# Performance work log

Measured on AMD Instinct MI355X. Metric: run time of the kernel, lower is better.

The kernel has to match this reference:

```python
import jax, jax.numpy as jnp
import numpy as np

N_EMBD = 768
N_HEAD = 12
HEAD_DIM = N_EMBD // N_HEAD


def setup_inputs() -> dict:
    key = jax.random.key(0)
    k1, k2, k3 = jax.random.split(key, 3)
    B, T = 8, 1024
    x = jax.random.normal(k1, (B, T, N_EMBD), dtype=jnp.float32)
    # torch Linear(n_embd, 3*n_embd, bias=False): y = x @ W^T; we store W_attn as (C, 3C)
    w_attn = jax.random.normal(k2, (N_EMBD, 3 * N_EMBD), dtype=jnp.float32) * (1.0 / np.sqrt(N_EMBD))
    w_proj = jax.random.normal(k3, (N_EMBD, N_EMBD), dtype=jnp.float32) * (1.0 / np.sqrt(N_EMBD))
    return {"x": x, "w_attn": w_attn, "w_proj": w_proj}


def reference(x, w_attn, w_proj):
    B, T, C = x.shape
    qkv = x @ w_attn                      # [B, T, 3C]
    q, k, v = jnp.split(qkv, 3, axis=-1)  # each [B, T, C]
    # [B, H, T, D]
    q = q.reshape(B, T, N_HEAD, HEAD_DIM).transpose(0, 2, 1, 3)
    k = k.reshape(B, T, N_HEAD, HEAD_DIM).transpose(0, 2, 1, 3)
    v = v.reshape(B, T, N_HEAD, HEAD_DIM).transpose(0, 2, 1, 3)
    scale = 1.0 / np.sqrt(HEAD_DIM)
    att = jnp.einsum('bhqd,bhkd->bhqk', q, k) * scale  # [B, H, T, T]
    causal = jnp.tril(jnp.ones((T, T), dtype=bool))
    att = jnp.where(causal[None, None, :, :], att, jnp.float32(-jnp.inf))
    att = jax.nn.softmax(att, axis=-1)
    # dropout disabled (eval / p=0.0) for deterministic reference
    y = jnp.einsum('bhqk,bhkd->bhqd', att, v)          # [B, H, T, D]
    y = y.transpose(0, 2, 1, 3).reshape(B, T, C)
    return y @ w_proj
```

## Files before the change

### kernel.cpp

```cpp
#include <hip/hip_runtime.h>
#include <hip/hip_bf16.h>
#include <math.h>

constexpr int Bz = 8;
constexpr int Tt = 1024;
constexpr int Cc = 768;
constexpr int Hh = 12;
constexpr int Dd = 64;
constexpr int BT = Bz * Tt;
constexpr int C3 = 3 * Cc;

using bf16x8 = __attribute__((ext_vector_type(8))) short;
using bf16x4 = __attribute__((ext_vector_type(4))) short;
using u16x8  = __attribute__((ext_vector_type(8))) unsigned short;
using f32x4  = __attribute__((ext_vector_type(4))) float;

__device__ __forceinline__ unsigned short f2bf(float f) {
  unsigned int u = __builtin_bit_cast(unsigned int, f);
  u += 0x7fffu + ((u >> 16) & 1u);
  return (unsigned short)(u >> 16);
}
__device__ __forceinline__ short f2bf_hw(float f) {
  __hip_bfloat16 h = __float2bfloat16(f);
  return __builtin_bit_cast(short, h);
}
__device__ __forceinline__ float fast_exp2(float x) {
#if __has_builtin(__builtin_amdgcn_exp2f)
  return __builtin_amdgcn_exp2f(x);
#else
  return exp2f(x);
#endif
}
__device__ __forceinline__ f32x4 mfma16_bf16(bf16x4 a, bf16x4 b, f32x4 c) {
#if __has_builtin(__builtin_amdgcn_mfma_f32_16x16x16bf16_1k)
  return __builtin_amdgcn_mfma_f32_16x16x16bf16_1k(a, b, c, 0, 0, 0);
#else
  asm volatile("v_mfma_f32_16x16x16_bf16 %0, %1, %2, %0" : "+v"(c) : "v"(a), "v"(b));
  return c;
#endif
}
__device__ __forceinline__ void stage16(const unsigned short* g, unsigned short* l) {
  __builtin_amdgcn_global_load_lds(
      (const __attribute__((address_space(1))) void*)g,
      (__attribute__((address_space(3))) void*)l, 16, 0, 0);
}

__global__ __launch_bounds__(256) void xcast_kernel(
    const float* __restrict__ in, unsigned short* __restrict__ out) {
  const size_t i = ((size_t)blockIdx.x * 256 + threadIdx.x) * 8;
  const float4 a = *(const float4*)(in + i);
  const float4 b = *(const float4*)(in + i + 4);
  u16x8 w;
  w[0] = f2bf(a.x); w[1] = f2bf(a.y); w[2] = f2bf(a.z); w[3] = f2bf(a.w);
  w[4] = f2bf(b.x); w[5] = f2bf(b.y); w[6] = f2bf(b.z); w[7] = f2bf(b.w);
  *(u16x8*)(out + i) = w;
}

__global__ __launch_bounds__(256) void tcast_kernel(
    const float* __restrict__ in, unsigned short* __restrict__ out, int K, int N) {
  __shared__ float t[32][33];
  const int tx = threadIdx.x, ty = threadIdx.y;
  const int kb = blockIdx.y * 32, nb = blockIdx.x * 32;
#pragma unroll
  for (int i = 0; i < 4; ++i)
    t[ty + 8 * i][tx] = in[(size_t)(kb + ty + 8 * i) * N + nb + tx];
  __syncthreads();
#pragma unroll
  for (int i = 0; i < 4; ++i)
    out[(size_t)(nb + ty + 8 * i) * K + kb + tx] = f2bf(t[tx][ty + 8 * i]);
}

#define GEMM_CORE_PROLOGUE()                                                   \
  __shared__ unsigned short As[128 * 32];                                      \
  __shared__ unsigned short Bs[128 * 32];                                      \
  const int tid = threadIdx.x;                                                 \
  const int wave = tid >> 6, lane = tid & 63;                                  \
  const int wr = wave >> 1, wc = wave & 1;                                     \
  const int lr = lane & 15;                                                    \
  const int lg = lane >> 4;                                                    \
  const int lrow = lane >> 2;                                                  \
  const int lcol = (lane & 3) * 8;                                             \
  const int brow = blockIdx.y * 128, bcol = blockIdx.x * 128;                  \
  f32x4 acc[4][4] = {};                                                        \
  for (int kt = 0; kt < K / 32; ++kt) {                                        \
    const int k0 = kt * 32;                                                    \
    __syncthreads();                                                           \
    _Pragma("unroll")                                                          \
    for (int i = 0; i < 2; ++i) {                                              \
      const int chunk = wave * 2 + i;                                          \
      const int row = chunk * 16 + lrow;                                       \
      stage16(A + (size_t)(brow + row) * K + k0 + lcol, &As[chunk * 512]);     \
      stage16(Bt + (size_t)(bcol + row) * K + k0 + lcol, &Bs[chunk * 512]);    \
    }                                                                          \
    __syncthreads();                                                           \
    bf16x8 af[4], bfr[4];                                                      \
    _Pragma("unroll")                                                          \
    for (int f = 0; f < 4; ++f) {                                              \
      af[f]  = *(const bf16x8*)&As[(wr * 64 + f * 16 + lr) * 32 + lg * 8];     \
      bfr[f] = *(const bf16x8*)&Bs[(wc * 64 + f * 16 + lr) * 32 + lg * 8];     \
    }                                                                          \
    _Pragma("unroll")                                                          \
    for (int fi = 0; fi < 4; ++fi)                                             \
      _Pragma("unroll")                                                        \
      for (int fj = 0; fj < 4; ++fj)                                           \
        acc[fi][fj] = __builtin_amdgcn_mfma_f32_16x16x32_bf16(                 \
            af[fi], bfr[fj], acc[fi][fj], 0, 0, 0);                            \
  }

__global__ __launch_bounds__(256) void gemm_qkv_kernel(
    const unsigned short* __restrict__ A, const unsigned short* __restrict__ Bt,
    unsigned short* __restrict__ qh, unsigned short* __restrict__ kh,
    unsigned short* __restrict__ vtg) {
  const int K = Cc;
  GEMM_CORE_PROLOGUE()

  const int region = bcol / Cc;
  const int nb = bcol - region * Cc;
#pragma unroll
  for (int fi = 0; fi < 4; ++fi) {
    const int m0 = brow + wr * 64 + fi * 16 + lg * 4;
    const int b_ = m0 >> 10, t0 = m0 & 1023;
#pragma unroll
    for (int fj = 0; fj < 4; ++fj) {
      const int n = nb + wc * 64 + fj * 16 + lr;
      const int h_ = n >> 6, d_ = n & 63;
      if (region < 2) {
        unsigned short* dst = (region == 0 ? qh : kh) +
            (((size_t)(b_ * Hh + h_)) * Tt + t0) * Dd + d_;
#pragma unroll
        for (int r = 0; r < 4; ++r) dst[(size_t)r * Dd] = f2bf(acc[fi][fj][r]);
      } else {
        ushort4 w;
        w.x = f2bf(acc[fi][fj][0]);
        w.y = f2bf(acc[fi][fj][1]);
        w.z = f2bf(acc[fi][fj][2]);
        w.w = f2bf(acc[fi][fj][3]);
        *(ushort4*)(vtg + (((size_t)(b_ * Hh + h_)) * Dd + d_) * Tt + t0) = w;
      }
    }
  }
}

__global__ __launch_bounds__(256) void gemm_bt_kernel(
    const unsigned short* __restrict__ A, const unsigned short* __restrict__ Bt,
    float* __restrict__ Cm, int M, int N, int K) {
  GEMM_CORE_PROLOGUE()

#pragma unroll
  for (int fi = 0; fi < 4; ++fi) {
    const size_t rbase = (size_t)(brow + wr * 64 + fi * 16 + lg * 4);
#pragma unroll
    for (int fj = 0; fj < 4; ++fj) {
      const int cbase = bcol + wc * 64 + fj * 16 + lr;
#pragma unroll
      for (int r = 0; r < 4; ++r)
        Cm[(rbase + r) * N + cbase] = acc[fi][fj][r];
    }
  }
}

__global__ __launch_bounds__(512, 4) void attn_mfma3_kernel(
    const unsigned short* __restrict__ qh, const unsigned short* __restrict__ kh,
    const unsigned short* __restrict__ vtg, unsigned short* __restrict__ y) {
  const int qtile = (Tt / 128 - 1) - blockIdx.x;
  const int h = blockIdx.y;
  const int b = blockIdx.z;
  const int qbase = qtile * 128;

  const int tid = threadIdx.x;
  const int wave = tid >> 6, lane = tid & 63;
  const int lr = lane & 15;
  const int lg = lane >> 4;

  __shared__ unsigned short Ks[128][72];
  __shared__ unsigned short Vt[64][136];

  const size_t head = ((size_t)(b * Hh + h)) * (Tt * Dd);
  const int qrow = qbase + wave * 16 + lr;

  bf16x8 qf0, qf1;
  {
    const unsigned short* qp = qh + head + (size_t)qrow * Dd;
    qf0 = *(const bf16x8*)(qp + lg * 8);
    qf1 = *(const bf16x8*)(qp + 32 + lg * 8);
  }

  f32x4 o[4] = {};
  float m_run = -INFINITY;
  float l_run = 0.0f;

  constexpr float kS = 0.125f * 1.4426950408889634f;
  const int lastT = qtile;

  {
    const unsigned short* kp = kh + head;
    const unsigned short* vp = vtg + head;
#pragma unroll
    for (int it = 0; it < 2; ++it) {
      const int s = tid + 512 * it;
      *(u16x8*)&Ks[s >> 3][(s & 7) * 8] =
          *(const u16x8*)(kp + (size_t)(s >> 3) * Dd + (s & 7) * 8);
      *(u16x8*)&Vt[s >> 4][(s & 15) * 8] =
          *(const u16x8*)(vp + (size_t)(s >> 4) * Tt + (s & 15) * 8);
    }
  }
  __syncthreads();

  for (int kt2 = 0; kt2 <= lastT; ++kt2) {
    const int kbase = kt2 * 128;
    const bool diagt = (kt2 == lastT);

    f32x4 sT[8];
#pragma unroll
    for (int jk = 0; jk < 8; ++jk) {
      if (!diagt || jk <= wave) {
        const bf16x8 kf0 = *(const bf16x8*)&Ks[jk * 16 + lr][lg * 8];
        const bf16x8 kf1 = *(const bf16x8*)&Ks[jk * 16 + lr][32 + lg * 8];
        f32x4 t = {};
        t = __builtin_amdgcn_mfma_f32_16x16x32_bf16(kf0, qf0, t, 0, 0, 0);
        t = __builtin_amdgcn_mfma_f32_16x16x32_bf16(kf1, qf1, t, 0, 0, 0);
        sT[jk] = t;
      }
    }

    u16x8 gk[2], gv[2];
    const bool havenext = (kt2 < lastT);
    if (havenext) {
      const unsigned short* kp = kh + head + (size_t)(kbase + 128) * Dd;
      const unsigned short* vp = vtg + head + (kbase + 128);
#pragma unroll
      for (int it = 0; it < 2; ++it) {
        const int s = tid + 512 * it;
        gk[it] = *(const u16x8*)(kp + (size_t)(s >> 3) * Dd + (s & 7) * 8);
        gv[it] = *(const u16x8*)(vp + (size_t)(s >> 4) * Tt + (s & 15) * 8);
      }
    }

    if (diagt) {
#pragma unroll
      for (int r = 0; r < 4; ++r) {
        const int k = kbase + wave * 16 + lg * 4 + r;
        if (k > qrow) sT[wave][r] = -INFINITY;
      }
    }

    float mx = -INFINITY;
#pragma unroll
    for (int jk = 0; jk < 8; ++jk) {
      if (!diagt || jk <= wave) {
        const float a0 = fmaxf(sT[jk][0], sT[jk][1]);
        const float a1 = fmaxf(sT[jk][2], sT[jk][3]);
        mx = fmaxf(mx, fmaxf(a0, a1));
      }
    }
    mx = fmaxf(mx, __shfl_xor(mx, 16));
    mx = fmaxf(mx, __shfl_xor(mx, 32));
    const float mnew = fmaxf(m_run, mx);
    const float mkS = mnew * kS;

    f32x4 lsv = {};
    bf16x4 pa[8];
#pragma unroll
    for (int jk = 0; jk < 8; ++jk) {
      if (!diagt || jk <= wave) {
        f32x4 p;
#pragma unroll
        for (int r = 0; r < 4; ++r)
          p[r] = fast_exp2(__builtin_fmaf(sT[jk][r], kS, -mkS));
        lsv += p;
        pa[jk][0] = f2bf_hw(p[0]); pa[jk][1] = f2bf_hw(p[1]);
        pa[jk][2] = f2bf_hw(p[2]); pa[jk][3] = f2bf_hw(p[3]);
      }
    }
    float ls = (lsv[0] + lsv[1]) + (lsv[2] + lsv[3]);
    ls += __shfl_xor(ls, 16);
    ls += __shfl_xor(ls, 32);

    const float alpha = fast_exp2((m_run - mnew) * kS);
    l_run = l_run * alpha + ls;
    m_run = mnew;
#pragma unroll
    for (int jd = 0; jd < 4; ++jd)
#pragma unroll
      for (int r = 0; r < 4; ++r) o[jd][r] *= alpha;

#pragma unroll
    for (int jk = 0; jk < 8; ++jk) {
      if (!diagt || jk <= wave) {
#pragma unroll
        for (int jd = 0; jd < 4; ++jd) {
          const bf16x4 vtf = *(const bf16x4*)&Vt[jd * 16 + lr][jk * 16 + lg * 4];
          o[jd] = mfma16_bf16(vtf, pa[jk], o[jd]);
        }
      }
    }

    __syncthreads();
    if (havenext) {
#pragma unroll
      for (int it = 0; it < 2; ++it) {
        const int s = tid + 512 * it;
        *(u16x8*)&Ks[s >> 3][(s & 7) * 8] = gk[it];
        *(u16x8*)&Vt[s >> 4][(s & 15) * 8] = gv[it];
      }
      __syncthreads();
    }
  }

  const float inv = 1.0f / l_run;
  unsigned short* yp = y + (size_t)(b * Tt + qrow) * Cc + h * Dd;
#pragma unroll
  for (int jd = 0; jd < 4; ++jd) {
    ushort4 w;
    w.x = (unsigned short)f2bf_hw(o[jd][0] * inv);
    w.y = (unsigned short)f2bf_hw(o[jd][1] * inv);
    w.z = (unsigned short)f2bf_hw(o[jd][2] * inv);
    w.w = (unsigned short)f2bf_hw(o[jd][3] * inv);
    *(ushort4*)(yp + jd * 16 + lg * 4) = w;
  }
}

extern "C" void kernel_launch(void* const* d_in, const int* in_sizes, int n_in,
                              void* d_out, int out_size, void* d_ws, size_t ws_size,
                              hipStream_t stream) {
  const float* x = (const float*)d_in[0];
  const float* w_attn = (const float*)d_in[1];
  const float* w_proj = (const float*)d_in[2];
  float* out = (float*)d_out;

  const size_t headTD = (size_t)Bz * Hh * Tt * Dd;
  unsigned short* xb   = (unsigned short*)d_ws;
  unsigned short* qh   = xb + (size_t)BT * Cc;
  unsigned short* kh   = qh + headTD;
  unsigned short* vtg  = kh + headTD;
  unsigned short* yatt = vtg + headTD;
  unsigned short* waT  = yatt + (size_t)BT * Cc;
  unsigned short* wpT  = waT + (size_t)C3 * Cc;

  xcast_kernel<<<(BT * Cc) / (256 * 8), 256, 0, stream>>>(x, xb);
  tcast_kernel<<<dim3(C3 / 32, Cc / 32), dim3(32, 8), 0, stream>>>(w_attn, waT, Cc, C3);
  tcast_kernel<<<dim3(Cc / 32, Cc / 32), dim3(32, 8), 0, stream>>>(w_proj, wpT, Cc, Cc);

  gemm_qkv_kernel<<<dim3(C3 / 128, BT / 128), 256, 0, stream>>>(xb, waT, qh, kh, vtg);

  attn_mfma3_kernel<<<dim3(Tt / 128, Hh, Bz), 512, 0, stream>>>(qh, kh, vtg, yatt);

  gemm_bt_kernel<<<dim3(Cc / 128, BT / 128), 256, 0, stream>>>(
      yatt, wpT, out, BT, Cc, Cc);
}
```

Before: 216.7 us.

## Pair 64-row causal query tiles per block for balanced attention work

The attention kernel now runs 256-thread blocks that each process two 64-row query tiles, a late one and an early one (15-pair and pair). This evens out the causal triangle's work across blocks instead of giving each 128-row block an unequal number of key tiles. The grid is reordered so batch-head is the fast dimension. MFMA sections are wrapped in s_setprio to favour matrix issue. K/V tiles are reloaded from the start for the second half, and the smaller blocks carry fewer waves to hide latency.

```diff
diff --git a/kernel.cpp b/kernel.cpp
--- a/kernel.cpp
+++ b/kernel.cpp
@@ -159,13 +159,12 @@
   }
 }
 
-__global__ __launch_bounds__(512, 4) void attn_mfma3_kernel(
+__global__ __launch_bounds__(256, 4) void attn_mfma4_kernel(
     const unsigned short* __restrict__ qh, const unsigned short* __restrict__ kh,
     const unsigned short* __restrict__ vtg, unsigned short* __restrict__ y) {
-  const int qtile = (Tt / 128 - 1) - blockIdx.x;
-  const int h = blockIdx.y;
-  const int b = blockIdx.z;
-  const int qbase = qtile * 128;
+  const int bh = blockIdx.x;
+  const int pair = blockIdx.y;
+  const int b = bh / Hh, h = bh % Hh;
 
   const int tid = threadIdx.x;
   const int wave = tid >> 6, lane = tid & 63;
@@ -175,148 +174,157 @@
   __shared__ unsigned short Ks[128][72];
   __shared__ unsigned short Vt[64][136];
 
-  const size_t head = ((size_t)(b * Hh + h)) * (Tt * Dd);
-  const int qrow = qbase + wave * 16 + lr;
-
-  bf16x8 qf0, qf1;
-  {
+  const size_t head = (size_t)bh * (Tt * Dd);
+  constexpr float kS = 0.125f * 1.4426950408889634f;
+
+#pragma unroll
+  for (int half = 0; half < 2; ++half) {
+    const int qt = (half == 0) ? (15 - pair) : pair;
+    const int qbase = qt * 64;
+    const int qrow = qbase + wave * 16 + lr;
+    const int lastT = qt >> 1;
+    const int relo = (qt & 1) * 4;
+
     const unsigned short* qp = qh + head + (size_t)qrow * Dd;
-    qf0 = *(const bf16x8*)(qp + lg * 8);
-    qf1 = *(const bf16x8*)(qp + 32 + lg * 8);
-  }
-
-  f32x4 o[4] = {};
-  float m_run = -INFINITY;
-  float l_run = 0.0f;
-
-  constexpr float kS = 0.125f * 1.4426950408889634f;
-  const int lastT = qtile;
-
-  {
-    const unsigned short* kp = kh + head;
-    const unsigned short* vp = vtg + head;
-#pragma unroll
-    for (int it = 0; it < 2; ++it) {
-      const int s = tid + 512 * it;
-      *(u16x8*)&Ks[s >> 3][(s & 7) * 8] =
-          *(const u16x8*)(kp + (size_t)(s >> 3) * Dd + (s & 7) * 8);
-      *(u16x8*)&Vt[s >> 4][(s & 15) * 8] =
-          *(const u16x8*)(vp + (size_t)(s >> 4) * Tt + (s & 15) * 8);
-    }
-  }
-  __syncthreads();
-
-  for (int kt2 = 0; kt2 <= lastT; ++kt2) {
-    const int kbase = kt2 * 128;
-    const bool diagt = (kt2 == lastT);
-
-    f32x4 sT[8];
-#pragma unroll
-    for (int jk = 0; jk < 8; ++jk) {
-      if (!diagt || jk <= wave) {
-        const bf16x8 kf0 = *(const bf16x8*)&Ks[jk * 16 + lr][lg * 8];
-        const bf16x8 kf1 = *(const bf16x8*)&Ks[jk * 16 + lr][32 + lg * 8];
-        f32x4 t = {};
-        t = __builtin_amdgcn_mfma_f32_16x16x32_bf16(kf0, qf0, t, 0, 0, 0);
-        t = __builtin_amdgcn_mfma_f32_16x16x32_bf16(kf1, qf1, t, 0, 0, 0);
-        sT[jk] = t;
-      }
-    }
-
-    u16x8 gk[2], gv[2];
-    const bool havenext = (kt2 < lastT);
-    if (havenext) {
-      const unsigned short* kp = kh + head + (size_t)(kbase + 128) * Dd;
-      const unsigned short* vp = vtg + head + (kbase + 128);
-#pragma unroll
-      for (int it = 0; it < 2; ++it) {
-        const int s = tid + 512 * it;
-        gk[it] = *(const u16x8*)(kp + (size_t)(s >> 3) * Dd + (s & 7) * 8);
-        gv[it] = *(const u16x8*)(vp + (size_t)(s >> 4) * Tt + (s & 15) * 8);
-      }
-    }
-
-    if (diagt) {
-#pragma unroll
-      for (int r = 0; r < 4; ++r) {
-        const int k = kbase + wave * 16 + lg * 4 + r;
-        if (k > qrow) sT[wave][r] = -INFINITY;
-      }
-    }
-
-    float mx = -INFINITY;
-#pragma unroll
-    for (int jk = 0; jk < 8; ++jk) {
-      if (!diagt || jk <= wave) {
-        const float a0 = fmaxf(sT[jk][0], sT[jk][1]);
-        const float a1 = fmaxf(sT[jk][2], sT[jk][3]);
-        mx = fmaxf(mx, fmaxf(a0, a1));
-      }
-    }
-    mx = fmaxf(mx, __shfl_xor(mx, 16));
-    mx = fmaxf(mx, __shfl_xor(mx, 32));
-    const float mnew = fmaxf(m_run, mx);
-    const float mkS = mnew * kS;
-
-    f32x4 lsv = {};
-    bf16x4 pa[8];
-#pragma unroll
-    for (int jk = 0; jk < 8; ++jk) {
-      if (!diagt || jk <= wave) {
-        f32x4 p;
-#pragma unroll
-        for (int r = 0; r < 4; ++r)
-          p[r] = fast_exp2(__builtin_fmaf(sT[jk][r], kS, -mkS));
-        lsv += p;
-        pa[jk][0] = f2bf_hw(p[0]); pa[jk][1] = f2bf_hw(p[1]);
-        pa[jk][2] = f2bf_hw(p[2]); pa[jk][3] = f2bf_hw(p[3]);
-      }
-    }
-    float ls = (lsv[0] + lsv[1]) + (lsv[2] + lsv[3]);
-    ls += __shfl_xor(ls, 16);
-    ls += __shfl_xor(ls, 32);
-
-    const float alpha = fast_exp2((m_run - mnew) * kS);
-    l_run = l_run * alpha + ls;
-    m_run = mnew;
-#pragma unroll
-    for (int jd = 0; jd < 4; ++jd)
-#pragma unroll
-      for (int r = 0; r < 4; ++r) o[jd][r] *= alpha;
-
-#pragma unroll
-    for (int jk = 0; jk < 8; ++jk) {
-      if (!diagt || jk <= wave) {
-#pragma unroll
-        for (int jd = 0; jd < 4; ++jd) {
-          const bf16x4 vtf = *(const bf16x4*)&Vt[jd * 16 + lr][jk * 16 + lg * 4];
-          o[jd] = mfma16_bf16(vtf, pa[jk], o[jd]);
-        }
-      }
-    }
+    const bf16x8 qf0 = *(const bf16x8*)(qp + lg * 8);
+    const bf16x8 qf1 = *(const bf16x8*)(qp + 32 + lg * 8);
+
+    f32x4 o[4] = {};
+    float m_run = -INFINITY;
+    float l_run = 0.0f;
 
     __syncthreads();
-    if (havenext) {
-#pragma unroll
-      for (int it = 0; it < 2; ++it) {
-        const int s = tid + 512 * it;
-        *(u16x8*)&Ks[s >> 3][(s & 7) * 8] = gk[it];
-        *(u16x8*)&Vt[s >> 4][(s & 15) * 8] = gv[it];
-      }
+    {
+      const unsigned short* kp = kh + head;
+      const unsigned short* vp = vtg + head;
+#pragma unroll
+      for (int it = 0; it < 4; ++it) {
+        const int s = tid + 256 * it;
+        *(u16x8*)&Ks[s >> 3][(s & 7) * 8] =
+            *(const u16x8*)(kp + (size_t)(s >> 3) * Dd + (s & 7) * 8);
+        *(u16x8*)&Vt[s >> 4][(s & 15) * 8] =
+            *(const u16x8*)(vp + (size_t)(s >> 4) * Tt + (s & 15) * 8);
+      }
+    }
+    __syncthreads();
+
+    for (int kt2 = 0; kt2 <= lastT; ++kt2) {
+      const int kbase = kt2 * 128;
+      const bool diagt = (kt2 == lastT);
+      const int jklim = diagt ? (relo + wave) : 7;
+
+      f32x4 sT[8];
+      __builtin_amdgcn_s_setprio(1);
+#pragma unroll
+      for (int jk = 0; jk < 8; ++jk) {
+        if (jk <= jklim) {
+          const bf16x8 kf0 = *(const bf16x8*)&Ks[jk * 16 + lr][lg * 8];
+          const bf16x8 kf1 = *(const bf16x8*)&Ks[jk * 16 + lr][32 + lg * 8];
+          f32x4 t = {};
+          t = __builtin_amdgcn_mfma_f32_16x16x32_bf16(kf0, qf0, t, 0, 0, 0);
+          t = __builtin_amdgcn_mfma_f32_16x16x32_bf16(kf1, qf1, t, 0, 0, 0);
+          sT[jk] = t;
+        }
+      }
+      __builtin_amdgcn_s_setprio(0);
+
+      u16x8 gk[4], gv[4];
+      const bool havenext = (kt2 < lastT);
+      if (havenext) {
+        const unsigned short* kp = kh + head + (size_t)(kbase + 128) * Dd;
+        const unsigned short* vp = vtg + head + (kbase + 128);
+#pragma unroll
+        for (int it = 0; it < 4; ++it) {
+          const int s = tid + 256 * it;
+          gk[it] = *(const u16x8*)(kp + (size_t)(s >> 3) * Dd + (s & 7) * 8);
+          gv[it] = *(const u16x8*)(vp + (size_t)(s >> 4) * Tt + (s & 15) * 8);
+        }
+      }
+
+      if (diagt) {
+#pragma unroll
+        for (int r = 0; r < 4; ++r) {
+          const int k = kbase + (relo + wave) * 16 + lg * 4 + r;
+          if (k > qrow) sT[relo + wave][r] = -INFINITY;
+        }
+      }
+
+      float mx = -INFINITY;
+#pragma unroll
+      for (int jk = 0; jk < 8; ++jk) {
+        if (jk <= jklim) {
+          const float a0 = fmaxf(sT[jk][0], sT[jk][1]);
+          const float a1 = fmaxf(sT[jk][2], sT[jk][3]);
+          mx = fmaxf(mx, fmaxf(a0, a1));
+        }
+      }
+      mx = fmaxf(mx, __shfl_xor(mx, 16));
+      mx = fmaxf(mx, __shfl_xor(mx, 32));
+      const float mnew = fmaxf(m_run, mx);
+      const float mkS = mnew * kS;
+
+      f32x4 lsv = {};
+      bf16x4 pa[8];
+#pragma unroll
+      for (int jk = 0; jk < 8; ++jk) {
+        if (jk <= jklim) {
+          f32x4 p;
+#pragma unroll
+          for (int r = 0; r < 4; ++r)
+            p[r] = fast_exp2(__builtin_fmaf(sT[jk][r], kS, -mkS));
+          lsv += p;
+          pa[jk][0] = f2bf_hw(p[0]); pa[jk][1] = f2bf_hw(p[1]);
+          pa[jk][2] = f2bf_hw(p[2]); pa[jk][3] = f2bf_hw(p[3]);
+        }
+      }
+      float ls = (lsv[0] + lsv[1]) + (lsv[2] + lsv[3]);
+      ls += __shfl_xor(ls, 16);
+      ls += __shfl_xor(ls, 32);
+
+      const float alpha = fast_exp2((m_run - mnew) * kS);
+      l_run = l_run * alpha + ls;
+      m_run = mnew;
+#pragma unroll
+      for (int jd = 0; jd < 4; ++jd)
+#pragma unroll
+        for (int r = 0; r < 4; ++r) o[jd][r] *= alpha;
+
+      __builtin_amdgcn_s_setprio(1);
+#pragma unroll
+      for (int jk = 0; jk < 8; ++jk) {
+        if (jk <= jklim) {
+#pragma unroll
+          for (int jd = 0; jd < 4; ++jd) {
+            const bf16x4 vtf = *(const bf16x4*)&Vt[jd * 16 + lr][jk * 16 + lg * 4];
+            o[jd] = mfma16_bf16(vtf, pa[jk], o[jd]);
+          }
+        }
+      }
+      __builtin_amdgcn_s_setprio(0);
+
       __syncthreads();
-    }
-  }
-
-  const float inv = 1.0f / l_run;
-  unsigned short* yp = y + (size_t)(b * Tt + qrow) * Cc + h * Dd;
-#pragma unroll
-  for (int jd = 0; jd < 4; ++jd) {
-    ushort4 w;
-    w.x = (unsigned short)f2bf_hw(o[jd][0] * inv);
-    w.y = (unsigned short)f2bf_hw(o[jd][1] * inv);
-    w.z = (unsigned short)f2bf_hw(o[jd][2] * inv);
-    w.w = (unsigned short)f2bf_hw(o[jd][3] * inv);
-    *(ushort4*)(yp + jd * 16 + lg * 4) = w;
+      if (havenext) {
+#pragma unroll
+        for (int it = 0; it < 4; ++it) {
+          const int s = tid + 256 * it;
+          *(u16x8*)&Ks[s >> 3][(s & 7) * 8] = gk[it];
+          *(u16x8*)&Vt[s >> 4][(s & 15) * 8] = gv[it];
+        }
+        __syncthreads();
+      }
+    }
+
+    const float inv = 1.0f / l_run;
+    unsigned short* yp = y + (size_t)(b * Tt + qrow) * Cc + h * Dd;
+#pragma unroll
+    for (int jd = 0; jd < 4; ++jd) {
+      ushort4 w;
+      w.x = (unsigned short)f2bf_hw(o[jd][0] * inv);
+      w.y = (unsigned short)f2bf_hw(o[jd][1] * inv);
+      w.z = (unsigned short)f2bf_hw(o[jd][2] * inv);
+      w.w = (unsigned short)f2bf_hw(o[jd][3] * inv);
+      *(ushort4*)(yp + jd * 16 + lg * 4) = w;
+    }
   }
 }
 
@@ -343,7 +351,7 @@
 
   gemm_qkv_kernel<<<dim3(C3 / 128, BT / 128), 256, 0, stream>>>(xb, waT, qh, kh, vtg);
 
-  attn_mfma3_kernel<<<dim3(Tt / 128, Hh, Bz), 512, 0, stream>>>(qh, kh, vtg, yatt);
+  attn_mfma4_kernel<<<dim3(Bz * Hh, 8), 256, 0, stream>>>(qh, kh, vtg, yatt);
 
   gemm_bt_kernel<<<dim3(Cc / 128, BT / 128), 256, 0, stream>>>(
       yatt, wpT, out, BT, Cc, Cc);
```

After: 236.9 us. +9.3%, slower.

## Fuse cast/transpose prep kernels into one launch and swizzle GEMM block mapping

Applied to the files above, without the earlier changes.

Merges the input cast kernel and the two weight transpose-cast kernels into a single prep kernel that dispatches on block index, cutting two kernel launches and their gaps. It also remaps GEMM block indices with an XCD-aware swizzle, so that consecutive blocks scheduled on the same chiplet share rows and columns for better L2 reuse. The swizzle assumes the block count is divisible by 8. In the combined kernel the transpose blocks carry shared memory they do not all need, and the branch adds some divergence.

```diff
diff --git a/kernel.cpp b/kernel.cpp
--- a/kernel.cpp
+++ b/kernel.cpp
@@ -45,29 +45,44 @@
       (__attribute__((address_space(3))) void*)l, 16, 0, 0);
 }
 
-__global__ __launch_bounds__(256) void xcast_kernel(
-    const float* __restrict__ in, unsigned short* __restrict__ out) {
-  const size_t i = ((size_t)blockIdx.x * 256 + threadIdx.x) * 8;
-  const float4 a = *(const float4*)(in + i);
-  const float4 b = *(const float4*)(in + i + 4);
-  u16x8 w;
-  w[0] = f2bf(a.x); w[1] = f2bf(a.y); w[2] = f2bf(a.z); w[3] = f2bf(a.w);
-  w[4] = f2bf(b.x); w[5] = f2bf(b.y); w[6] = f2bf(b.z); w[7] = f2bf(b.w);
-  *(u16x8*)(out + i) = w;
-}
-
-__global__ __launch_bounds__(256) void tcast_kernel(
-    const float* __restrict__ in, unsigned short* __restrict__ out, int K, int N) {
+__global__ __launch_bounds__(256) void prep_kernel(
+    const float* __restrict__ x, unsigned short* __restrict__ xb,
+    const float* __restrict__ w_attn, unsigned short* __restrict__ waT,
+    const float* __restrict__ w_proj, unsigned short* __restrict__ wpT) {
   __shared__ float t[32][33];
-  const int tx = threadIdx.x, ty = threadIdx.y;
-  const int kb = blockIdx.y * 32, nb = blockIdx.x * 32;
-#pragma unroll
-  for (int i = 0; i < 4; ++i)
-    t[ty + 8 * i][tx] = in[(size_t)(kb + ty + 8 * i) * N + nb + tx];
-  __syncthreads();
-#pragma unroll
-  for (int i = 0; i < 4; ++i)
-    out[(size_t)(nb + ty + 8 * i) * K + kb + tx] = f2bf(t[tx][ty + 8 * i]);
+  const int blk = blockIdx.x;
+  const int tid = threadIdx.x;
+  if (blk < 3072) {
+    const size_t i = ((size_t)blk * 256 + tid) * 8;
+    const float4 a = *(const float4*)(x + i);
+    const float4 b = *(const float4*)(x + i + 4);
+    u16x8 w;
+    w[0] = f2bf(a.x); w[1] = f2bf(a.y); w[2] = f2bf(a.z); w[3] = f2bf(a.w);
+    w[4] = f2bf(b.x); w[5] = f2bf(b.y); w[6] = f2bf(b.z); w[7] = f2bf(b.w);
+    *(u16x8*)(xb + i) = w;
+  } else {
+    const float* in;
+    unsigned short* out;
+    int K, N, bx, by;
+    if (blk < 3072 + 1728) {
+      const int b2 = blk - 3072;
+      in = w_attn; out = waT; K = Cc; N = C3;
+      bx = b2 % 72; by = b2 / 72;
+    } else {
+      const int b3 = blk - (3072 + 1728);
+      in = w_proj; out = wpT; K = Cc; N = Cc;
+      bx = b3 % 24; by = b3 / 24;
+    }
+    const int tx = tid & 31, ty = tid >> 5;
+    const int kb = by * 32, nb = bx * 32;
+#pragma unroll
+    for (int i = 0; i < 4; ++i)
+      t[ty + 8 * i][tx] = in[(size_t)(kb + ty + 8 * i) * N + nb + tx];
+    __syncthreads();
+#pragma unroll
+    for (int i = 0; i < 4; ++i)
+      out[(size_t)(nb + ty + 8 * i) * K + kb + tx] = f2bf(t[tx][ty + 8 * i]);
+  }
 }
 
 #define GEMM_CORE_PROLOGUE()                                                   \
@@ -80,7 +95,11 @@
   const int lg = lane >> 4;                                                    \
   const int lrow = lane >> 2;                                                  \
   const int lcol = (lane & 3) * 8;                                             \
-  const int brow = blockIdx.y * 128, bcol = blockIdx.x * 128;                  \
+  const int nx = gridDim.x;                                                    \
+  const int lin = blockIdx.x + nx * blockIdx.y;                                \
+  const int cpx = (nx * gridDim.y) >> 3;                                       \
+  const int swz = (lin & 7) * cpx + (lin >> 3);                                \
+  const int brow = (swz / nx) * 128, bcol = (swz % nx) * 128;                  \
   f32x4 acc[4][4] = {};                                                        \
   for (int kt = 0; kt < K / 32; ++kt) {                                        \
     const int k0 = kt * 32;                                                    \
@@ -337,9 +356,8 @@
   unsigned short* waT  = yatt + (size_t)BT * Cc;
   unsigned short* wpT  = waT + (size_t)C3 * Cc;
 
-  xcast_kernel<<<(BT * Cc) / (256 * 8), 256, 0, stream>>>(x, xb);
-  tcast_kernel<<<dim3(C3 / 32, Cc / 32), dim3(32, 8), 0, stream>>>(w_attn, waT, Cc, C3);
-  tcast_kernel<<<dim3(Cc / 32, Cc / 32), dim3(32, 8), 0, stream>>>(w_proj, wpT, Cc, Cc);
+  prep_kernel<<<3072 + 1728 + 576, 256, 0, stream>>>(
+      x, xb, w_attn, waT, w_proj, wpT);
 
   gemm_qkv_kernel<<<dim3(C3 / 128, BT / 128), 256, 0, stream>>>(xb, waT, qh, kh, vtg);
 
```

After: 207.8 us. 1.04x faster.
